# Kernel tuning notes

Hardware: AMD Instinct MI355X
Metric: run time of the kernel (lower is better)

Reference implementation:

```python
import jax, jax.numpy as jnp
import numpy as np

N = 50000
E = 1600000
IN_C, HID_C, OUT_C, EDGE_D = 128, 64, 64, 32
NEG_SLOPE = 0.2


def _add_self_loops(edge_index, edge_attr, n):
    # PyG add_self_loops with fill_value='mean': loop attr = mean of incoming edge attrs per node
    src, dst = edge_index[0], edge_index[1]
    attr_sum = jax.ops.segment_sum(edge_attr, dst, num_segments=n)          # [N, D]
    cnt = jax.ops.segment_sum(jnp.ones((edge_attr.shape[0],), edge_attr.dtype), dst, num_segments=n)
    loop_attr = attr_sum / jnp.maximum(cnt, 1.0)[:, None]                   # [N, D]
    loop = jnp.arange(n, dtype=src.dtype)
    src = jnp.concatenate([src, loop])
    dst = jnp.concatenate([dst, loop])
    edge_attr = jnp.concatenate([edge_attr, loop_attr], axis=0)
    return src, dst, edge_attr


def gat_conv(x, edge_index, edge_attr, W, We, att_src, att_dst, att_edge, bias, n):
    # heads=1, concat=True (PyG defaults); att_* have shape [1, C]
    src, dst, ea = _add_self_loops(edge_index, edge_attr, n)
    h = x @ W                                   # [N, C]
    a_src = jnp.sum(h * att_src, axis=-1)       # [N]
    a_dst = jnp.sum(h * att_dst, axis=-1)       # [N]
    he = ea @ We                                # [E+N, C]
    a_edge = jnp.sum(he * att_edge, axis=-1)    # [E+N]
    alpha = a_src[src] + a_dst[dst] + a_edge
    alpha = jax.nn.leaky_relu(alpha, NEG_SLOPE)
    # segment softmax over destination nodes (every node has a self-loop)
    m = jax.ops.segment_max(alpha, dst, num_segments=n)
    alpha = jnp.exp(alpha - m[dst])
    denom = jax.ops.segment_sum(alpha, dst, num_segments=n)
    alpha = alpha / (denom[dst] + 1e-16)
    out = jax.ops.segment_sum(alpha[:, None] * h[src], dst, num_segments=n)  # [N, C]
    return out + bias


def setup_inputs() -> dict:
    key = jax.random.key(0)
    ks = jax.random.split(key, 12)
    def g(k, shape, scale=1.0):
        return jax.random.normal(k, shape, dtype=jnp.float32) * scale
    x = g(ks[0], (N, IN_C))
    edge_index = jax.random.randint(ks[1], (2, E), 0, N, dtype=jnp.int64)
    edge_attr = g(ks[2], (E, EDGE_D))
    s1 = 1.0 / np.sqrt(IN_C)
    s2 = 1.0 / np.sqrt(HID_C)
    se = 1.0 / np.sqrt(EDGE_D)
    return {
        "x": x, "edge_index": edge_index, "edge_attr": edge_attr,
        "W1": g(ks[3], (IN_C, HID_C), s1), "We1": g(ks[4], (EDGE_D, HID_C), se),
        "att_src1": g(ks[5], (1, HID_C), s2), "att_dst1": g(ks[6], (1, HID_C), s2),
        "att_edge1": g(ks[7], (1, HID_C), s2), "b1": jnp.zeros((HID_C,), jnp.float32),
        "W2": g(ks[8], (HID_C, OUT_C), s2), "We2": g(ks[9], (EDGE_D, OUT_C), se),
        "att_src2": g(ks[10], (1, OUT_C), s2), "att_dst2": g(ks[11], (1, OUT_C), s2),
        "att_edge2": g(jax.random.fold_in(key, 99), (1, OUT_C), s2),
        "b2": jnp.zeros((OUT_C,), jnp.float32),
    }


def reference(x, edge_index, edge_attr,
              W1, We1, att_src1, att_dst1, att_edge1, b1,
              W2, We2, att_src2, att_dst2, att_edge2, b2):
    h = gat_conv(x, edge_index, edge_attr, W1, We1, att_src1, att_dst1, att_edge1, b1, N)
    h = jax.nn.relu(h)
    # F.dropout(p=0.1, training=self.training): identity in eval mode
    out = gat_conv(h, edge_index, edge_attr, W2, We2, att_src2, att_dst2, att_edge2, b2, N)
    return out
```

## Files before the change

### kernel.cpp

```cpp
#include <hip/hip_runtime.h>
#include <hip/hip_bf16.h>

__global__ __launch_bounds__(256)
void zero_kernel(int* __restrict__ p, int n) {
    int i = blockIdx.x * 256 + threadIdx.x;
    if (i < n) p[i] = 0;
}

__global__ void we_kernel(const float* __restrict__ We1, const float* __restrict__ ae1v,
                          const float* __restrict__ We2, const float* __restrict__ ae2v,
                          float* __restrict__ we1, float* __restrict__ we2) {
    int t = threadIdx.x;
    const float* W = (t < 32) ? We1 : We2;
    const float* a = (t < 32) ? ae1v : ae2v;
    float* o       = (t < 32) ? we1 : we2;
    int k = t & 31;
    float s = 0.f;
    for (int c = 0; c < 64; ++c) s += W[k * 64 + c] * a[c];
    o[k] = s;
}

__global__ __launch_bounds__(256)
void edge_pass_kernel(const float4* __restrict__ ea, const int* __restrict__ eidx,
                      const float* __restrict__ we1g, const float* __restrict__ we2g,
                      int* __restrict__ cnt, float4* __restrict__ s_tmp, int E) {
    __shared__ float w1s[32], w2s[32];
    if (threadIdx.x < 32) w1s[threadIdx.x] = we1g[threadIdx.x];
    else if (threadIdx.x < 64) w2s[threadIdx.x - 32] = we2g[threadIdx.x - 32];
    __syncthreads();
    int e = blockIdx.x * 256 + threadIdx.x;
    if (e >= E) return;
    float acc1 = 0.f, acc2 = 0.f;
#pragma unroll
    for (int q = 0; q < 8; ++q) {
        float4 v = ea[(size_t)e * 8 + q];
        acc1 += v.x * w1s[q * 4 + 0] + v.y * w1s[q * 4 + 1] +
                v.z * w1s[q * 4 + 2] + v.w * w1s[q * 4 + 3];
        acc2 += v.x * w2s[q * 4 + 0] + v.y * w2s[q * 4 + 1] +
                v.z * w2s[q * 4 + 2] + v.w * w2s[q * 4 + 3];
    }
    int src = eidx[e];
    int dst = eidx[E + e];
    int rk = atomicAdd(&cnt[dst], 1);
    unsigned packed = ((unsigned)rk << 16) | (unsigned)dst;
    s_tmp[e] = make_float4(acc1, acc2, __int_as_float(src),
                           __int_as_float((int)packed));
}

__global__ __launch_bounds__(256)
void scanA_kernel(const int* __restrict__ cnt, int* __restrict__ bsum, int n) {
    int idx = blockIdx.x * 256 + threadIdx.x;
    int v = (idx < n) ? cnt[idx] : 0;
#pragma unroll
    for (int off = 32; off >= 1; off >>= 1) v += __shfl_xor(v, off, 64);
    __shared__ int ws[4];
    int lane = threadIdx.x & 63, wid = threadIdx.x >> 6;
    if (lane == 0) ws[wid] = v;
    __syncthreads();
    if (threadIdx.x == 0) bsum[blockIdx.x] = ws[0] + ws[1] + ws[2] + ws[3];
}

__global__ void scanB_kernel(const int* __restrict__ bsum, int* __restrict__ boff, int nb) {
    int lane = threadIdx.x;
    int carry = 0;
    for (int base = 0; base < nb; base += 64) {
        int idx = base + lane;
        int v = (idx < nb) ? bsum[idx] : 0;
        int s = v;
#pragma unroll
        for (int off = 1; off < 64; off <<= 1) {
            int t = __shfl_up(s, off, 64);
            if (lane >= off) s += t;
        }
        if (idx < nb) boff[idx] = carry + s - v;
        carry += __shfl(s, 63, 64);
    }
}

__global__ __launch_bounds__(256)
void scanC_kernel(const int* __restrict__ cnt, const int* __restrict__ boff,
                  int* __restrict__ row_ptr, int n, int E) {
    __shared__ int ws[4];
    __shared__ int woff[4];
    int idx = blockIdx.x * 256 + threadIdx.x;
    int lane = threadIdx.x & 63, wid = threadIdx.x >> 6;
    int v = (idx < n) ? cnt[idx] : 0;
    int s = v;
#pragma unroll
    for (int off = 1; off < 64; off <<= 1) {
        int t = __shfl_up(s, off, 64);
        if (lane >= off) s += t;
    }
    if (lane == 63) ws[wid] = s;
    __syncthreads();
    if (threadIdx.x == 0) {
        int run = 0;
        for (int w = 0; w < 4; ++w) { int t = ws[w]; woff[w] = run; run += t; }
    }
    __syncthreads();
    if (idx < n) row_ptr[idx] = boff[blockIdx.x] + woff[wid] + s - v;
    if (idx == 0) row_ptr[n] = E;
}

__global__ __launch_bounds__(256)
void scatter_kernel(const float4* __restrict__ s_tmp, const int* __restrict__ row_ptr,
                    float4* __restrict__ s_rec, int E) {
    int e = blockIdx.x * 256 + threadIdx.x;
    if (e >= E) return;
    float4 r = s_tmp[e];
    unsigned packed = (unsigned)__float_as_int(r.w);
    int dst = (int)(packed & 0xFFFFu);
    int rk  = (int)(packed >> 16);
    int pos = row_ptr[dst] + rk;
    s_rec[pos] = make_float4(r.x, r.y, r.z, 0.f);
}

template <int INC>
__global__ __launch_bounds__(256)
void gemm_kernel(const float* __restrict__ X, const float* __restrict__ W,
                 const float* __restrict__ asv, const float* __restrict__ adv,
                 __hip_bfloat16* __restrict__ H, float* __restrict__ a_src,
                 float* __restrict__ a_dst, int n) {
    __shared__ float Wl[INC * 64];
    for (int t = threadIdx.x; t < INC * 64; t += 256) Wl[t] = W[t];
    __syncthreads();
    int wid = threadIdx.x >> 6, lane = threadIdx.x & 63;
    int i = blockIdx.x * 4 + wid;
    if (i >= n) return;
    const float4* xr = (const float4*)(X + (size_t)i * INC);
    float acc = 0.f;
#pragma unroll
    for (int k4 = 0; k4 < INC / 4; ++k4) {
        float4 xv = xr[k4];
        acc += xv.x * Wl[(k4 * 4 + 0) * 64 + lane];
        acc += xv.y * Wl[(k4 * 4 + 1) * 64 + lane];
        acc += xv.z * Wl[(k4 * 4 + 2) * 64 + lane];
        acc += xv.w * Wl[(k4 * 4 + 3) * 64 + lane];
    }
    H[(size_t)i * 64 + lane] = __float2bfloat16(acc);
    float s = acc * asv[lane];
    float d = acc * adv[lane];
#pragma unroll
    for (int off = 32; off >= 1; off >>= 1) {
        s += __shfl_xor(s, off, 64);
        d += __shfl_xor(d, off, 64);
    }
    if (lane == 0) { a_src[i] = s; a_dst[i] = d; }
}

__device__ __forceinline__ float4 bf4_to_f4(ushort4 u) {
    float4 f;
    f.x = __uint_as_float((unsigned)u.x << 16);
    f.y = __uint_as_float((unsigned)u.y << 16);
    f.z = __uint_as_float((unsigned)u.z << 16);
    f.w = __uint_as_float((unsigned)u.w << 16);
    return f;
}

template <int AEIDX, bool RELU>
__global__ __launch_bounds__(256)
void agg_fused_kernel(const int* __restrict__ row_ptr, const float4* __restrict__ s_rec,
                      const float* __restrict__ a_srcv, const float* __restrict__ a_dstv,
                      const ushort4* __restrict__ H4, const float* __restrict__ bias,
                      float* __restrict__ out, int n) {
    int wid = threadIdx.x >> 6, lane = threadIdx.x & 63;
    int i = blockIdx.x * 4 + wid;
    if (i >= n) return;
    int start = row_ptr[i], end = row_ptr[i + 1];
    int deg = end - start;
    float adst = a_dstv[i];

    float al0 = -INFINITY, al1 = -INFINITY;
    int src0 = 0, src1 = 0;
    float aeloc = 0.f;
    {
        int j = start + lane;
        if (j < end) {
            float4 r = s_rec[j];
            float ae = (AEIDX == 0) ? r.x : r.y;
            src0 = __float_as_int(r.z);
            float a = a_srcv[src0] + adst + ae;
            al0 = a > 0.f ? a : 0.2f * a;
            aeloc += ae;
        }
    }
    if (deg > 64) {
        int j = start + 64 + lane;
        if (j < end) {
            float4 r = s_rec[j];
            float ae = (AEIDX == 0) ? r.x : r.y;
            src1 = __float_as_int(r.z);
            float a = a_srcv[src1] + adst + ae;
            al1 = a > 0.f ? a : 0.2f * a;
            aeloc += ae;
        }
    }
    float mloc = fmaxf(al0, al1);
    for (int base = start + 128; base < end; base += 64) {
        int j = base + lane;
        if (j < end) {
            float4 r = s_rec[j];
            float ae = (AEIDX == 0) ? r.x : r.y;
            int s = __float_as_int(r.z);
            float a = a_srcv[s] + adst + ae;
            a = a > 0.f ? a : 0.2f * a;
            mloc = fmaxf(mloc, a);
            aeloc += ae;
        }
    }
#pragma unroll
    for (int off = 32; off >= 1; off >>= 1) {
        mloc = fmaxf(mloc, __shfl_xor(mloc, off, 64));
        aeloc += __shfl_xor(aeloc, off, 64);
    }
    float ael = aeloc / (float)(deg > 0 ? deg : 1);
    float als = a_srcv[i] + adst + ael;
    als = als > 0.f ? als : 0.2f * als;
    float m = fmaxf(mloc, als);

    float w0 = (start + lane < end)      ? __expf(al0 - m) : 0.f;
    float w1 = (start + 64 + lane < end) ? __expf(al1 - m) : 0.f;
    float dloc = w0 + w1;
    for (int base = start + 128; base < end; base += 64) {
        int j = base + lane;
        if (j < end) {
            float4 r = s_rec[j];
            float ae = (AEIDX == 0) ? r.x : r.y;
            int s = __float_as_int(r.z);
            float a = a_srcv[s] + adst + ae;
            a = a > 0.f ? a : 0.2f * a;
            dloc += __expf(a - m);
        }
    }
#pragma unroll
    for (int off = 32; off >= 1; off >>= 1) dloc += __shfl_xor(dloc, off, 64);
    float wself = __expf(als - m);
    float inv = 1.f / (dloc + wself + 1e-16f);

    int sub = lane >> 4;
    int c4  = lane & 15;
    float4 acc = make_float4(0.f, 0.f, 0.f, 0.f);
    int mainCnt = deg < 128 ? deg : 128;
    for (int r = 0; r < mainCnt; r += 4) {
        int rel = r + sub;
        float wa = __shfl(w0, rel & 63, 64);
        float wb = __shfl(w1, rel & 63, 64);
        int   sa = __shfl(src0, rel & 63, 64);
        int   sb = __shfl(src1, rel & 63, 64);
        float w = (rel < 64) ? wa : wb;
        int   s = (rel < 64) ? sa : sb;
        float4 hv = bf4_to_f4(H4[(size_t)s * 16 + c4]);
        acc.x += w * hv.x; acc.y += w * hv.y;
        acc.z += w * hv.z; acc.w += w * hv.w;
    }
    for (int j = start + 128; j < end; j += 4) {
        int jj = j + sub;
        if (jj < end) {
            float4 r = s_rec[jj];
            float ae = (AEIDX == 0) ? r.x : r.y;
            int s = __float_as_int(r.z);
            float a = a_srcv[s] + adst + ae;
            a = a > 0.f ? a : 0.2f * a;
            float w = __expf(a - m);
            float4 hv = bf4_to_f4(H4[(size_t)s * 16 + c4]);
            acc.x += w * hv.x; acc.y += w * hv.y;
            acc.z += w * hv.z; acc.w += w * hv.w;
        }
    }
#pragma unroll
    for (int off = 16; off <= 32; off <<= 1) {
        acc.x += __shfl_xor(acc.x, off, 64);
        acc.y += __shfl_xor(acc.y, off, 64);
        acc.z += __shfl_xor(acc.z, off, 64);
        acc.w += __shfl_xor(acc.w, off, 64);
    }
    float4 hv = bf4_to_f4(H4[(size_t)i * 16 + c4]);
    float4 bv = ((const float4*)bias)[c4];
    float4 o;
    o.x = (acc.x + wself * hv.x) * inv + bv.x;
    o.y = (acc.y + wself * hv.y) * inv + bv.y;
    o.z = (acc.z + wself * hv.z) * inv + bv.z;
    o.w = (acc.w + wself * hv.w) * inv + bv.w;
    if (RELU) {
        o.x = fmaxf(o.x, 0.f); o.y = fmaxf(o.y, 0.f);
        o.z = fmaxf(o.z, 0.f); o.w = fmaxf(o.w, 0.f);
    }
    if (sub == 0) ((float4*)out)[(size_t)i * 16 + c4] = o;
}

extern "C" void kernel_launch(void* const* d_in, const int* in_sizes, int n_in,
                              void* d_out, int out_size, void* d_ws, size_t ws_size,
                              hipStream_t stream) {
    const float* x        = (const float*)d_in[0];
    const int*   eidx     = (const int*)d_in[1];
    const float* eattr    = (const float*)d_in[2];
    const float* W1       = (const float*)d_in[3];
    const float* We1      = (const float*)d_in[4];
    const float* att_src1 = (const float*)d_in[5];
    const float* att_dst1 = (const float*)d_in[6];
    const float* att_edge1= (const float*)d_in[7];
    const float* b1       = (const float*)d_in[8];
    const float* W2       = (const float*)d_in[9];
    const float* We2      = (const float*)d_in[10];
    const float* att_src2 = (const float*)d_in[11];
    const float* att_dst2 = (const float*)d_in[12];
    const float* att_edge2= (const float*)d_in[13];
    const float* b2       = (const float*)d_in[14];
    float* out = (float*)d_out;

    const int n = in_sizes[0] / 128;
    const int E = in_sizes[1] / 2;

    char* ws = (char*)d_ws;
    size_t off = 0;
    auto carve = [&](size_t bytes) {
        char* p = ws + off;
        off = (off + bytes + 255) & ~(size_t)255;
        return p;
    };
    const int nblkScan = (n + 255) / 256;
    float*  we1    = (float*)carve(32 * 4);
    float*  we2    = (float*)carve(32 * 4);
    int*    cnt    = (int*)carve((size_t)n * 4);
    int*    bsum   = (int*)carve((size_t)nblkScan * 4);
    int*    boff   = (int*)carve((size_t)nblkScan * 4);
    int*    row_ptr= (int*)carve((size_t)(n + 1) * 4);
    float4* s_tmp  = (float4*)carve((size_t)E * 16);
    float4* s_rec  = (float4*)carve((size_t)E * 16);
    __hip_bfloat16* bufA = (__hip_bfloat16*)carve((size_t)n * 64 * 2);
    float*  bufB   = (float*)carve((size_t)n * 64 * 4);
    float*  a_src  = (float*)carve((size_t)n * 4);
    float*  a_dst  = (float*)carve((size_t)n * 4);

    zero_kernel<<<nblkScan, 256, 0, stream>>>(cnt, n);

    we_kernel<<<1, 64, 0, stream>>>(We1, att_edge1, We2, att_edge2, we1, we2);

    int egrid = (E + 255) / 256;
    edge_pass_kernel<<<egrid, 256, 0, stream>>>((const float4*)eattr, eidx,
                                                we1, we2, cnt, s_tmp, E);
    scanA_kernel<<<nblkScan, 256, 0, stream>>>(cnt, bsum, n);
    scanB_kernel<<<1, 64, 0, stream>>>(bsum, boff, nblkScan);
    scanC_kernel<<<nblkScan, 256, 0, stream>>>(cnt, boff, row_ptr, n, E);

    scatter_kernel<<<egrid, 256, 0, stream>>>(s_tmp, row_ptr, s_rec, E);

    int ngrid = (n + 3) / 4;
    gemm_kernel<128><<<ngrid, 256, 0, stream>>>(x, W1, att_src1, att_dst1,
                                                bufA, a_src, a_dst, n);
    agg_fused_kernel<0, true><<<ngrid, 256, 0, stream>>>(row_ptr, s_rec, a_src,
                                                         a_dst, (const ushort4*)bufA,
                                                         b1, bufB, n);
    gemm_kernel<64><<<ngrid, 256, 0, stream>>>(bufB, W2, att_src2, att_dst2,
                                               bufA, a_src, a_dst, n);
    agg_fused_kernel<1, false><<<ngrid, 256, 0, stream>>>(row_ptr, s_rec, a_src,
                                                          a_dst, (const ushort4*)bufA,
                                                          b2, out, n);
}
```

Before: 328.2 us.

## Pack edge records to 8 bytes with bf16 scores and coalesce edge pass

Edge records shrink from a 16-byte float4 to an 8-byte uint2 holding the source index and two bf16 edge-attention scores. Scatter metadata moves to a separate 4-byte array, so the scatter and aggregation passes move less data. The edge pass now gives each edge eight threads that each read one float4 and reduce with shuffles, which coalesces the edge_attr reads. Aggregation stages source and weight pairs in shared memory instead of per-iteration shuffles, at the cost of bf16 rounding on the edge scores.

```diff
diff --git a/kernel.cpp b/kernel.cpp
--- a/kernel.cpp
+++ b/kernel.cpp
@@ -1,5 +1,16 @@
 #include <hip/hip_runtime.h>
 #include <hip/hip_bf16.h>
+
+__device__ __forceinline__ unsigned f2bf_rne(float f) {
+    unsigned u = __float_as_uint(f);
+    u += 0x7FFFu + ((u >> 16) & 1u);
+    return u >> 16;
+}
+__device__ __forceinline__ float bf_lo(unsigned p) { return __uint_as_float(p << 16); }
+__device__ __forceinline__ float bf_hi(unsigned p) { return __uint_as_float(p & 0xFFFF0000u); }
+template <int I> __device__ __forceinline__ float bfsel(unsigned p) {
+    return (I == 0) ? bf_lo(p) : bf_hi(p);
+}
 
 __global__ __launch_bounds__(256)
 void zero_kernel(int* __restrict__ p, int n) {
@@ -23,28 +34,29 @@
 __global__ __launch_bounds__(256)
 void edge_pass_kernel(const float4* __restrict__ ea, const int* __restrict__ eidx,
                       const float* __restrict__ we1g, const float* __restrict__ we2g,
-                      int* __restrict__ cnt, float4* __restrict__ s_tmp, int E) {
-    __shared__ float w1s[32], w2s[32];
-    if (threadIdx.x < 32) w1s[threadIdx.x] = we1g[threadIdx.x];
-    else if (threadIdx.x < 64) w2s[threadIdx.x - 32] = we2g[threadIdx.x - 32];
-    __syncthreads();
-    int e = blockIdx.x * 256 + threadIdx.x;
+                      int* __restrict__ cnt, uint2* __restrict__ pack8,
+                      unsigned* __restrict__ meta, int E) {
+    int tid = threadIdx.x;
+    int q = tid & 7;
+    int e = blockIdx.x * 32 + (tid >> 3);
     if (e >= E) return;
-    float acc1 = 0.f, acc2 = 0.f;
-#pragma unroll
-    for (int q = 0; q < 8; ++q) {
-        float4 v = ea[(size_t)e * 8 + q];
-        acc1 += v.x * w1s[q * 4 + 0] + v.y * w1s[q * 4 + 1] +
-                v.z * w1s[q * 4 + 2] + v.w * w1s[q * 4 + 3];
-        acc2 += v.x * w2s[q * 4 + 0] + v.y * w2s[q * 4 + 1] +
-                v.z * w2s[q * 4 + 2] + v.w * w2s[q * 4 + 3];
-    }
-    int src = eidx[e];
-    int dst = eidx[E + e];
-    int rk = atomicAdd(&cnt[dst], 1);
-    unsigned packed = ((unsigned)rk << 16) | (unsigned)dst;
-    s_tmp[e] = make_float4(acc1, acc2, __int_as_float(src),
-                           __int_as_float((int)packed));
+    float4 w1 = ((const float4*)we1g)[q];
+    float4 w2 = ((const float4*)we2g)[q];
+    float4 v = ea[(size_t)e * 8 + q];
+    float a1 = v.x * w1.x + v.y * w1.y + v.z * w1.z + v.w * w1.w;
+    float a2 = v.x * w2.x + v.y * w2.y + v.z * w2.z + v.w * w2.w;
+#pragma unroll
+    for (int off = 1; off < 8; off <<= 1) {
+        a1 += __shfl_xor(a1, off, 64);
+        a2 += __shfl_xor(a2, off, 64);
+    }
+    if (q == 0) {
+        int src = eidx[e];
+        int dst = eidx[E + e];
+        int rk = atomicAdd(&cnt[dst], 1);
+        pack8[e] = make_uint2((unsigned)src, f2bf_rne(a1) | (f2bf_rne(a2) << 16));
+        meta[e] = ((unsigned)rk << 16) | (unsigned)dst;
+    }
 }
 
 __global__ __launch_bounds__(256)
@@ -103,16 +115,14 @@
 }
 
 __global__ __launch_bounds__(256)
-void scatter_kernel(const float4* __restrict__ s_tmp, const int* __restrict__ row_ptr,
-                    float4* __restrict__ s_rec, int E) {
+void scatter_kernel(const uint2* __restrict__ pack8, const unsigned* __restrict__ meta,
+                    const int* __restrict__ row_ptr, uint2* __restrict__ s_rec, int E) {
     int e = blockIdx.x * 256 + threadIdx.x;
     if (e >= E) return;
-    float4 r = s_tmp[e];
-    unsigned packed = (unsigned)__float_as_int(r.w);
-    int dst = (int)(packed & 0xFFFFu);
-    int rk  = (int)(packed >> 16);
-    int pos = row_ptr[dst] + rk;
-    s_rec[pos] = make_float4(r.x, r.y, r.z, 0.f);
+    unsigned m = meta[e];
+    int dst = (int)(m & 0xFFFFu);
+    int rk  = (int)(m >> 16);
+    s_rec[row_ptr[dst] + rk] = pack8[e];
 }
 
 template <int INC>
@@ -159,10 +169,11 @@
 
 template <int AEIDX, bool RELU>
 __global__ __launch_bounds__(256)
-void agg_fused_kernel(const int* __restrict__ row_ptr, const float4* __restrict__ s_rec,
+void agg_fused_kernel(const int* __restrict__ row_ptr, const uint2* __restrict__ s_rec,
                       const float* __restrict__ a_srcv, const float* __restrict__ a_dstv,
                       const ushort4* __restrict__ H4, const float* __restrict__ bias,
                       float* __restrict__ out, int n) {
+    __shared__ uint2 wl[4][128];
     int wid = threadIdx.x >> 6, lane = threadIdx.x & 63;
     int i = blockIdx.x * 4 + wid;
     if (i >= n) return;
@@ -176,9 +187,9 @@
     {
         int j = start + lane;
         if (j < end) {
-            float4 r = s_rec[j];
-            float ae = (AEIDX == 0) ? r.x : r.y;
-            src0 = __float_as_int(r.z);
+            uint2 r = s_rec[j];
+            float ae = bfsel<AEIDX>(r.y);
+            src0 = (int)r.x;
             float a = a_srcv[src0] + adst + ae;
             al0 = a > 0.f ? a : 0.2f * a;
             aeloc += ae;
@@ -187,9 +198,9 @@
     if (deg > 64) {
         int j = start + 64 + lane;
         if (j < end) {
-            float4 r = s_rec[j];
-            float ae = (AEIDX == 0) ? r.x : r.y;
-            src1 = __float_as_int(r.z);
+            uint2 r = s_rec[j];
+            float ae = bfsel<AEIDX>(r.y);
+            src1 = (int)r.x;
             float a = a_srcv[src1] + adst + ae;
             al1 = a > 0.f ? a : 0.2f * a;
             aeloc += ae;
@@ -199,9 +210,9 @@
     for (int base = start + 128; base < end; base += 64) {
         int j = base + lane;
         if (j < end) {
-            float4 r = s_rec[j];
-            float ae = (AEIDX == 0) ? r.x : r.y;
-            int s = __float_as_int(r.z);
+            uint2 r = s_rec[j];
+            float ae = bfsel<AEIDX>(r.y);
+            int s = (int)r.x;
             float a = a_srcv[s] + adst + ae;
             a = a > 0.f ? a : 0.2f * a;
             mloc = fmaxf(mloc, a);
@@ -224,9 +235,9 @@
     for (int base = start + 128; base < end; base += 64) {
         int j = base + lane;
         if (j < end) {
-            float4 r = s_rec[j];
-            float ae = (AEIDX == 0) ? r.x : r.y;
-            int s = __float_as_int(r.z);
+            uint2 r = s_rec[j];
+            float ae = bfsel<AEIDX>(r.y);
+            int s = (int)r.x;
             float a = a_srcv[s] + adst + ae;
             a = a > 0.f ? a : 0.2f * a;
             dloc += __expf(a - m);
@@ -236,29 +247,28 @@
     for (int off = 32; off >= 1; off >>= 1) dloc += __shfl_xor(dloc, off, 64);
     float wself = __expf(als - m);
     float inv = 1.f / (dloc + wself + 1e-16f);
+
+    wl[wid][lane]      = make_uint2((unsigned)src0, __float_as_uint(w0));
+    wl[wid][64 + lane] = make_uint2((unsigned)src1, __float_as_uint(w1));
 
     int sub = lane >> 4;
     int c4  = lane & 15;
     float4 acc = make_float4(0.f, 0.f, 0.f, 0.f);
     int mainCnt = deg < 128 ? deg : 128;
+#pragma unroll 4
     for (int r = 0; r < mainCnt; r += 4) {
-        int rel = r + sub;
-        float wa = __shfl(w0, rel & 63, 64);
-        float wb = __shfl(w1, rel & 63, 64);
-        int   sa = __shfl(src0, rel & 63, 64);
-        int   sb = __shfl(src1, rel & 63, 64);
-        float w = (rel < 64) ? wa : wb;
-        int   s = (rel < 64) ? sa : sb;
-        float4 hv = bf4_to_f4(H4[(size_t)s * 16 + c4]);
+        uint2 sw = wl[wid][r + sub];
+        float w = __uint_as_float(sw.y);
+        float4 hv = bf4_to_f4(H4[(size_t)sw.x * 16 + c4]);
         acc.x += w * hv.x; acc.y += w * hv.y;
         acc.z += w * hv.z; acc.w += w * hv.w;
     }
     for (int j = start + 128; j < end; j += 4) {
         int jj = j + sub;
         if (jj < end) {
-            float4 r = s_rec[jj];
-            float ae = (AEIDX == 0) ? r.x : r.y;
-            int s = __float_as_int(r.z);
+            uint2 r = s_rec[jj];
+            float ae = bfsel<AEIDX>(r.y);
+            int s = (int)r.x;
             float a = a_srcv[s] + adst + ae;
             a = a > 0.f ? a : 0.2f * a;
             float w = __expf(a - m);
@@ -319,31 +329,31 @@
         return p;
     };
     const int nblkScan = (n + 255) / 256;
-    float*  we1    = (float*)carve(32 * 4);
-    float*  we2    = (float*)carve(32 * 4);
-    int*    cnt    = (int*)carve((size_t)n * 4);
-    int*    bsum   = (int*)carve((size_t)nblkScan * 4);
-    int*    boff   = (int*)carve((size_t)nblkScan * 4);
-    int*    row_ptr= (int*)carve((size_t)(n + 1) * 4);
-    float4* s_tmp  = (float4*)carve((size_t)E * 16);
-    float4* s_rec  = (float4*)carve((size_t)E * 16);
+    float*    we1    = (float*)carve(32 * 4);
+    float*    we2    = (float*)carve(32 * 4);
+    int*      cnt    = (int*)carve((size_t)n * 4);
+    int*      bsum   = (int*)carve((size_t)nblkScan * 4);
+    int*      boff   = (int*)carve((size_t)nblkScan * 4);
+    int*      row_ptr= (int*)carve((size_t)(n + 1) * 4);
+    uint2*    pack8  = (uint2*)carve((size_t)E * 8);
+    unsigned* meta   = (unsigned*)carve((size_t)E * 4);
+    uint2*    s_rec  = (uint2*)carve((size_t)E * 8);
     __hip_bfloat16* bufA = (__hip_bfloat16*)carve((size_t)n * 64 * 2);
-    float*  bufB   = (float*)carve((size_t)n * 64 * 4);
-    float*  a_src  = (float*)carve((size_t)n * 4);
-    float*  a_dst  = (float*)carve((size_t)n * 4);
+    float*    bufB   = (float*)carve((size_t)n * 64 * 4);
+    float*    a_src  = (float*)carve((size_t)n * 4);
+    float*    a_dst  = (float*)carve((size_t)n * 4);
 
     zero_kernel<<<nblkScan, 256, 0, stream>>>(cnt, n);
 
     we_kernel<<<1, 64, 0, stream>>>(We1, att_edge1, We2, att_edge2, we1, we2);
 
-    int egrid = (E + 255) / 256;
-    edge_pass_kernel<<<egrid, 256, 0, stream>>>((const float4*)eattr, eidx,
-                                                we1, we2, cnt, s_tmp, E);
+    edge_pass_kernel<<<(E + 31) / 32, 256, 0, stream>>>((const float4*)eattr, eidx,
+                                                        we1, we2, cnt, pack8, meta, E);
     scanA_kernel<<<nblkScan, 256, 0, stream>>>(cnt, bsum, n);
     scanB_kernel<<<1, 64, 0, stream>>>(bsum, boff, nblkScan);
     scanC_kernel<<<nblkScan, 256, 0, stream>>>(cnt, boff, row_ptr, n, E);
 
-    scatter_kernel<<<egrid, 256, 0, stream>>>(s_tmp, row_ptr, s_rec, E);
+    scatter_kernel<<<(E + 255) / 256, 256, 0, stream>>>(pack8, meta, row_ptr, s_rec, E);
 
     int ngrid = (n + 3) / 4;
     gemm_kernel<128><<<ngrid, 256, 0, stream>>>(x, W1, att_src1, att_dst1,
```

Result: faster. 299.6 us (-8.7%).
